# Performance work log

Hardware: AMD Instinct MI355X
Metric: run time of the kernel (lower is better)

## Reference

```python
import jax, jax.numpy as jnp
import numpy as np

B, T, D, H = 2, 2048, 2048, 16
HD = D // H  # head_dim = 128
NEG = -1e9


def setup_inputs() -> dict:
    key = jax.random.key(0)
    k1, k2, k3 = jax.random.split(key, 3)
    x = jax.random.normal(k1, (B, T, D), dtype=jnp.float32)
    # additive causal mask: 0 on/below diagonal, large negative above
    mask = jnp.where(jnp.tril(jnp.ones((T, T), dtype=bool)), 0.0, NEG).astype(jnp.float32)
    causal_mask = mask[None, None]  # [1,1,T,T]
    w_qkv = jax.random.normal(k2, (3 * D, D), dtype=jnp.float32) * (D ** -0.5)
    w_out = jax.random.normal(k3, (D, D), dtype=jnp.float32) * (D ** -0.5)
    b_out = jnp.zeros((D,), dtype=jnp.float32)
    return {"x": x, "causal_mask": causal_mask, "w_qkv": w_qkv, "w_out": w_out, "b_out": b_out}


def reference(x, causal_mask, w_qkv, w_out, b_out):
    scale = HD ** -0.5
    qkv = jnp.einsum('btd,ed->bte', x, w_qkv)          # [B,T,3D]
    q, k, v = jnp.split(qkv, 3, axis=-1)
    def heads(t):  # [B,T,D] -> [B,H,T,HD]
        return t.reshape(B, T, H, HD).transpose(0, 2, 1, 3)
    q, k, v = heads(q), heads(k), heads(v)
    attn = jnp.einsum('bhqd,bhkd->bhqk', q, k) * scale + causal_mask
    attn = jax.nn.softmax(attn, axis=-1)
    out = jnp.einsum('bhqk,bhkd->bhqd', attn, v)       # [B,H,T,HD]
    out = out.transpose(0, 2, 1, 3).reshape(B, T, D)
    return jnp.einsum('btd,ed->bte', out, w_out) + b_out
```

## Files before the change

kernel.cpp:

```cpp
#include <hip/hip_runtime.h>
#include <stdint.h>

typedef uint16_t u16;
typedef __attribute__((ext_vector_type(8))) short short8;
typedef __attribute__((ext_vector_type(4))) float f32x4;
typedef __attribute__((ext_vector_type(16))) float f32x16;

#define MFMA16(a, b, c) __builtin_amdgcn_mfma_f32_16x16x32_bf16((a), (b), (c), 0, 0, 0)
#define MFMA32(a, b, c) __builtin_amdgcn_mfma_f32_32x32x16_bf16((a), (b), (c), 0, 0, 0)
#define AS1 __attribute__((address_space(1)))
#define AS3 __attribute__((address_space(3)))

__device__ __forceinline__ void gld_lds16(const u16* g, u16* l) {
  __builtin_amdgcn_global_load_lds((const AS1 void*)g, (AS3 void*)l, 16, 0, 0);
}

__device__ __forceinline__ u16 f2bf(float f) {
  uint32_t u = __float_as_uint(f);
  u += 0x7fffu + ((u >> 16) & 1u);
  return (u16)(u >> 16);
}

__global__ __launch_bounds__(256) void cvt_all(const float* __restrict__ x,
                                               const float* __restrict__ wqkv,
                                               const float* __restrict__ wout,
                                               u16* __restrict__ xb,
                                               u16* __restrict__ wqkvb,
                                               u16* __restrict__ woutb) {
  const int n1 = 8388608 / 4, n2 = 12582912 / 4;
  int i = blockIdx.x * 256 + threadIdx.x;
  const float* src;
  u16* dst;
  int j;
  if (i < n1) {
    src = x; dst = xb; j = i;
  } else if (i < n1 + n2) {
    src = wqkv; dst = wqkvb; j = i - n1;
  } else {
    src = wout; dst = woutb; j = i - n1 - n2;
  }
  float4 v = ((const float4*)src)[j];
  uint2 o;
  o.x = (uint32_t)f2bf(v.x) | ((uint32_t)f2bf(v.y) << 16);
  o.y = (uint32_t)f2bf(v.z) | ((uint32_t)f2bf(v.w) << 16);
  ((uint2*)dst)[j] = o;
}

template <int N>
__device__ __forceinline__ void bar_vm() {
  asm volatile("s_waitcnt vmcnt(%0)\n\ts_barrier" ::"n"(N) : "memory");
}
__device__ __forceinline__ void bar_fence() {
  asm volatile("s_barrier" ::: "memory");
}

__global__ __launch_bounds__(512, 2) void proj8_gemm(const u16* __restrict__ xb,
                                                     const u16* __restrict__ wqkvb,
                                                     u16* __restrict__ qkb) {
  constexpr int ASZ = 256 * 64;
  constexpr int NT = 32;
  __shared__ u16 sm[4 * ASZ];

  int bx = blockIdx.x;
  bx = (bx & 7) * 32 + (bx >> 3);
  const int mt = bx >> 4, nt = bx & 15;
  const u16* Ab = xb + (size_t)mt * 256 * 2048;
  const u16* Bb = wqkvb + (size_t)nt * 256 * 2048;
  u16* C = qkb + (size_t)mt * 256 * 4096 + nt * 256;

  const int tid = threadIdx.x, lane = tid & 63, w = tid >> 6;
  const int wm = w >> 2, wn = w & 3;
  const int lo = lane & 15, q4 = lane >> 4;

  f32x4 acc[8][4];
  const f32x4 fzero = {0.f, 0.f, 0.f, 0.f};
#pragma unroll
  for (int i = 0; i < 8; ++i)
#pragma unroll
    for (int j = 0; j < 4; ++j) acc[i][j] = fzero;

  auto stage_half = [&](int tau, int h) {
    const int slot = tau & 1;
    const int k0 = tau * 64;
    const u16* G = (h < 2) ? Bb : Ab;
    u16* L = sm + (h < 2 ? 2 * ASZ : 0) + slot * ASZ;
#pragma unroll
    for (int s = 0; s < 2; ++s) {
      const int c = tid + s * 512;
      const int hr = c >> 3, pc = c & 7;
      const int r = (h < 2) ? (h * 128 + hr)
                            : ((hr & 63) + ((hr >> 6) << 7) + ((h & 1) << 6));
      const int c4 = pc ^ (r & 7);
      gld_lds16(G + (size_t)r * 2048 + k0 + c4 * 8, L + r * 64 + pc * 8);
    }
  };

  stage_half(0, 0);
  stage_half(0, 1);
  stage_half(0, 2);
  stage_half(0, 3);
  bar_vm<2>();

  for (int tau = 0; tau < NT; ++tau) {
    const u16* As = sm + (tau & 1) * ASZ;
    const u16* Bs = sm + 2 * ASZ + (tau & 1) * ASZ;
    short8 bf[8];
#pragma unroll
    for (int q = 0; q < 4; ++q) {
      if (q == 0) {
#pragma unroll
        for (int j = 0; j < 4; ++j)
#pragma unroll
          for (int kk = 0; kk < 2; ++kk) {
            const int r = wn * 64 + j * 16 + lo;
            bf[j * 2 + kk] =
                *(const short8*)(Bs + r * 64 + (((kk * 4 + q4) ^ (r & 7)) * 8));
          }
      }
      short8 af[2][2];
#pragma unroll
      for (int i = 0; i < 2; ++i)
#pragma unroll
        for (int kk = 0; kk < 2; ++kk) {
          const int r = wm * 128 + q * 32 + i * 16 + lo;
          af[i][kk] =
              *(const short8*)(As + r * 64 + (((kk * 4 + q4) ^ (r & 7)) * 8));
        }
      if (tau + 1 < NT) stage_half(tau + 1, q);
      bar_fence();
      __builtin_amdgcn_s_setprio(1);
#pragma unroll
      for (int i = 0; i < 2; ++i)
#pragma unroll
        for (int j = 0; j < 4; ++j)
#pragma unroll
          for (int kk = 0; kk < 2; ++kk)
            acc[q * 2 + i][j] = MFMA16(af[i][kk], bf[j * 2 + kk], acc[q * 2 + i][j]);
      __builtin_amdgcn_s_setprio(0);
      if (q == 0) {
        if (tau == NT - 1) bar_vm<0>();
        else bar_vm<2>();
      } else if (q == 1) {
        bar_vm<4>();
      } else if (q == 2) {
        bar_vm<6>();
      } else {
        if (tau < NT - 1) bar_vm<2>();
      }
    }
  }

#pragma unroll
  for (int i = 0; i < 8; ++i)
#pragma unroll
    for (int j = 0; j < 4; ++j) {
      const int col = wn * 64 + j * 16 + lo;
#pragma unroll
      for (int e = 0; e < 4; ++e) {
        const int row = wm * 128 + i * 16 + q4 * 4 + e;
        C[(size_t)row * 4096 + col] = f2bf(acc[i][j][e]);
      }
    }
}

template <int MFR>
__device__ __forceinline__ void gemm_core3(const u16* __restrict__ Ab,
                                           const u16* __restrict__ Bb,
                                           u16* sm, int tid,
                                           f32x4 acc[MFR][4]) {
  constexpr int AROWS = MFR * 32;
  constexpr int ASZ = AROWS * 32;
  constexpr int BSZ = 128 * 32;
  constexpr int BUF = ASZ + BSZ;
  constexpr int NT = 64;
  constexpr int ALD = AROWS / 64;
  constexpr int VN = ALD + 2;

  const int lane = tid & 63, w = tid >> 6;
  const int wr = w >> 1, wc = w & 1;
  const int lo = lane & 15, q4 = lane >> 4;
  const int pcl = (((lo & 1) << 2) | q4) ^ ((lo >> 1) & 7);
  const int loff = (lo >> 1) * 64 + pcl * 8;

  auto stage = [&](int g) {
    u16* As = sm + (g % 3) * BUF;
    u16* Bs = As + ASZ;
    const int k0 = g * 32;
#pragma unroll
    for (int s = 0; s < ALD; ++s) {
      const int c = tid + s * 256;
      const int sr = c >> 3, pc = c & 7;
      const int t = pc ^ (sr & 7);
      const int r = sr * 2 + (t >> 2), c4 = t & 3;
      gld_lds16(Ab + (size_t)r * 2048 + k0 + c4 * 8, As + c * 8);
    }
#pragma unroll
    for (int s = 0; s < 2; ++s) {
      const int c = tid + s * 256;
      const int sr = c >> 3, pc = c & 7;
      const int t = pc ^ (sr & 7);
      const int r = sr * 2 + (t >> 2), c4 = t & 3;
      gld_lds16(Bb + (size_t)r * 2048 + k0 + c4 * 8, Bs + c * 8);
    }
  };

  stage(0);
  stage(1);
  bar_vm<VN>();

  for (int g = 0; g < NT; ++g) {
    const u16* As = sm + (g % 3) * BUF;
    const u16* Bs = As + ASZ;
    if (g + 2 < NT) stage(g + 2);
    short8 af[MFR], bf[4];
#pragma unroll
    for (int i = 0; i < MFR; ++i)
      af[i] = *(const short8*)(As + (wr * (MFR * 16) + i * 16) * 32 + loff);
#pragma unroll
    for (int j = 0; j < 4; ++j)
      bf[j] = *(const short8*)(Bs + (wc * 64 + j * 16) * 32 + loff);
    __builtin_amdgcn_s_setprio(1);
#pragma unroll
    for (int i = 0; i < MFR; ++i)
#pragma unroll
      for (int j = 0; j < 4; ++j) acc[i][j] = MFMA16(af[i], bf[j], acc[i][j]);
    __builtin_amdgcn_s_setprio(0);
    if (g + 1 < NT) {
      if (g + 2 < NT) {
        bar_vm<VN>();
      } else {
        bar_vm<0>();
      }
    }
  }
}

__global__ __launch_bounds__(256, 2) void vproj_gemm(const u16* __restrict__ wqkvb,
                                                     const u16* __restrict__ xb,
                                                     u16* __restrict__ vtb) {
  __shared__ u16 sm[3 * (256 * 32 + 128 * 32)];
  int bx = blockIdx.x;
  bx = (bx & 7) * 32 + (bx >> 3);
  const int tid = threadIdx.x;
  const int mt = bx >> 5, nt = bx & 31;
  const u16* Ab = wqkvb + (size_t)(4096 + mt * 256) * 2048;
  const u16* Bb = xb + (size_t)nt * 128 * 2048;
  u16* C = vtb + (size_t)mt * 256 * 4096 + nt * 128;
  f32x4 acc[8][4];
  const f32x4 fzero = {0.f, 0.f, 0.f, 0.f};
#pragma unroll
  for (int i = 0; i < 8; ++i)
#pragma unroll
    for (int j = 0; j < 4; ++j) acc[i][j] = fzero;

  gemm_core3<8>(Ab, Bb, sm, tid, acc);

  const int lane = tid & 63, w = tid >> 6;
  const int wr = w >> 1, wc = w & 1;
  const int lo = lane & 15, q4 = lane >> 4;
#pragma unroll
  for (int i = 0; i < 8; ++i)
#pragma unroll
    for (int j = 0; j < 4; ++j) {
      const int col = wc * 64 + j * 16 + lo;
#pragma unroll
      for (int e = 0; e < 4; ++e) {
        const int row = wr * 128 + i * 16 + q4 * 4 + e;
        C[(size_t)row * 4096 + col] = f2bf(acc[i][j][e]);
      }
    }
}

__global__ __launch_bounds__(256, 2) void out_gemm(const u16* __restrict__ A,
                                                   const u16* __restrict__ B,
                                                   float* __restrict__ Cf,
                                                   const float* __restrict__ bias) {
  __shared__ u16 sm[3 * (256 * 32 + 128 * 32)];
  int bx = blockIdx.x;
  bx = (bx & 7) * 32 + (bx >> 3);
  const int tid = threadIdx.x;
  const int mt = bx >> 4, nt = bx & 15;
  const u16* Ab = A + (size_t)mt * 256 * 2048;
  const u16* Bb = B + (size_t)nt * 128 * 2048;
  f32x4 acc[8][4];
  const f32x4 fzero = {0.f, 0.f, 0.f, 0.f};
#pragma unroll
  for (int i = 0; i < 8; ++i)
#pragma unroll
    for (int j = 0; j < 4; ++j) acc[i][j] = fzero;

  gemm_core3<8>(Ab, Bb, sm, tid, acc);

  const int lane = tid & 63, w = tid >> 6;
  const int wr = w >> 1, wc = w & 1;
  const int lo = lane & 15, q4 = lane >> 4;
#pragma unroll
  for (int i = 0; i < 8; ++i)
#pragma unroll
    for (int j = 0; j < 4; ++j) {
      const int col = nt * 128 + wc * 64 + j * 16 + lo;
      const float bv = bias[col];
#pragma unroll
      for (int e = 0; e < 4; ++e) {
        const int row = mt * 256 + wr * 128 + i * 16 + q4 * 4 + e;
        Cf[(size_t)row * 2048 + col] = acc[i][j][e] + bv;
      }
    }
}

__device__ __forceinline__ int swz(int r, int c) {
  return r * 128 + (c ^ (((r ^ (r >> 3)) & 7) << 4));
}

__global__ __launch_bounds__(512) void flash_attn(const u16* __restrict__ qk,
                                                  const u16* __restrict__ vt,
                                                  u16* __restrict__ aout) {
  constexpr int T = 2048, WQK = 4096, D = 2048;
  constexpr int TILE = 128 * 128;
  __shared__ u16 smem[5 * TILE];

  const int bx = blockIdx.x;
  const int p = bx >> 5;
  const int g = bx & 31;
  const int h = g & 15, b = g >> 4;
  const int tid = threadIdx.x, lane = tid & 63, w = tid >> 6;
  const int wr = w >> 1, wcc = w & 1;
  const int l31 = lane & 31, h5 = lane >> 5;

  const u16* Qb = qk + (size_t)b * T * WQK + h * 128;
  const u16* Kb = Qb + 2048;
  const u16* Vtb = vt + (size_t)h * 128 * 4096 + b * 2048;
  u16* Ps = smem + 4 * TILE;

  const float cexp = 0.08838834764831843f * 1.4426950408889634f;
  short8 onesf;
#pragma unroll
  for (int j = 0; j < 8; ++j) onesf[j] = (short)0x3F80;

  for (int half = 0; half < 2; ++half) {
    const int qt = half ? p : 15 - p;
    const int q0 = qt * 128;

    short8 qf[8];
#pragma unroll
    for (int kc = 0; kc < 8; ++kc)
      qf[kc] = *(const short8*)(Qb + (size_t)(q0 + wr * 32 + l31) * WQK +
                                kc * 16 + h5 * 8);

    f32x16 o[2], osum;
#pragma unroll
    for (int e = 0; e < 16; ++e) { o[0][e] = 0.f; o[1][e] = 0.f; osum[e] = 0.f; }

    __syncthreads();
#pragma unroll
    for (int s = 0; s < 4; ++s) {
      const int c = tid + s * 512, r = c >> 4, cc = c & 15;
      const int cs = cc ^ (((r ^ (r >> 3)) & 7) << 1);
      gld_lds16(Kb + (size_t)r * WQK + cs * 8, smem + c * 8);
      gld_lds16(Vtb + (size_t)r * 4096 + cs * 8, smem + 2 * TILE + c * 8);
    }

    for (int kt = 0; kt <= qt; ++kt) {
      const int curo = (kt & 1) * TILE, nxto = TILE - curo;
      __syncthreads();
      if (kt < qt) {
        const int k0n = (kt + 1) * 128;
#pragma unroll
        for (int s = 0; s < 4; ++s) {
          const int c = tid + s * 512, r = c >> 4, cc = c & 15;
          const int cs = cc ^ (((r ^ (r >> 3)) & 7) << 1);
          gld_lds16(Kb + (size_t)(k0n + r) * WQK + cs * 8, smem + nxto + c * 8);
          gld_lds16(Vtb + (size_t)r * 4096 + k0n + cs * 8,
                    smem + 2 * TILE + nxto + c * 8);
        }
      }

      const u16* Ksc = smem + curo;
      const u16* Vsc = smem + 2 * TILE + curo;

      f32x16 s2[2];
#pragma unroll
      for (int e = 0; e < 16; ++e) { s2[0][e] = 0.f; s2[1][e] = 0.f; }
#pragma unroll
      for (int kc = 0; kc < 8; ++kc)
#pragma unroll
        for (int ct = 0; ct < 2; ++ct) {
          short8 kf = *(const short8*)&Ksc[swz(wcc * 64 + ct * 32 + l31,
                                               kc * 16 + h5 * 8)];
          s2[ct] = MFMA32(qf[kc], kf, s2[ct]);
        }

      const bool diag = (kt == qt);
#pragma unroll
      for (int ct = 0; ct < 2; ++ct) {
        const int kcol = wcc * 64 + ct * 32 + l31;
#pragma unroll
        for (int reg = 0; reg < 16; ++reg) {
          const int qrow = wr * 32 + (reg & 3) + 8 * (reg >> 2) + 4 * h5;
          float pv = exp2f(s2[ct][reg] * cexp);
          if (diag && (kcol > qrow)) pv = 0.f;
          Ps[swz(qrow, kcol)] = f2bf(pv);
        }
      }
      asm volatile("s_waitcnt lgkmcnt(0)\n\ts_barrier" ::: "memory");

#pragma unroll
      for (int kc = 0; kc < 8; ++kc) {
        short8 pa = *(const short8*)&Ps[swz(wr * 32 + l31, kc * 16 + h5 * 8)];
        osum = MFMA32(pa, onesf, osum);
#pragma unroll
        for (int dt = 0; dt < 2; ++dt) {
          short8 vf = *(const short8*)&Vsc[swz(wcc * 64 + dt * 32 + l31,
                                               kc * 16 + h5 * 8)];
          o[dt] = MFMA32(pa, vf, o[dt]);
        }
      }
    }

#pragma unroll
    for (int reg = 0; reg < 16; ++reg) {
      const int row = q0 + wr * 32 + (reg & 3) + 8 * (reg >> 2) + 4 * h5;
      const float inv = 1.f / osum[reg];
#pragma unroll
      for (int dt = 0; dt < 2; ++dt)
        aout[(size_t)(b * T + row) * D + h * 128 + wcc * 64 + dt * 32 + l31] =
            f2bf(o[dt][reg] * inv);
    }
  }
}

extern "C" void kernel_launch(void* const* d_in, const int* in_sizes, int n_in,
                              void* d_out, int out_size, void* d_ws, size_t ws_size,
                              hipStream_t stream) {
  const float* x = (const float*)d_in[0];
  const float* w_qkv = (const float*)d_in[2];
  const float* w_out = (const float*)d_in[3];
  const float* b_out = (const float*)d_in[4];
  float* out = (float*)d_out;

  const int BT = 4096, D = 2048, D3 = 6144;
  u16* xb = (u16*)d_ws;
  u16* wqkvb = xb + (size_t)BT * D;
  u16* woutb = wqkvb + (size_t)D3 * D;
  u16* qkb = woutb + (size_t)D * D;
  u16* vtb = qkb + (size_t)BT * 4096;
  u16* attnb = vtb + (size_t)D * BT;

  const int total4 = (BT * D + D3 * D + D * D) / 4;
  cvt_all<<<total4 / 256, 256, 0, stream>>>(x, w_qkv, w_out, xb, wqkvb, woutb);
  proj8_gemm<<<256, 512, 0, stream>>>(xb, wqkvb, qkb);
  vproj_gemm<<<256, 256, 0, stream>>>(wqkvb, xb, vtb);
  flash_attn<<<256, 512, 0, stream>>>(qkb, vtb, attnb);
  out_gemm<<<256, 256, 0, stream>>>(attnb, woutb, out, b_out);
}
```

Baseline: 355.9 us.

## Keep softmax probabilities in registers, fold scale into Q projection, shrink GEMM tiles

```diff
diff --git a/kernel.cpp b/kernel.cpp
--- a/kernel.cpp
+++ b/kernel.cpp
@@ -150,6 +150,8 @@
     }
   }
 
+  const float sc =
+      (nt < 8) ? (0.08838834764831843f * 1.4426950408889634f) : 1.0f;
 #pragma unroll
   for (int i = 0; i < 8; ++i)
 #pragma unroll
@@ -158,7 +160,7 @@
 #pragma unroll
       for (int e = 0; e < 4; ++e) {
         const int row = wm * 128 + i * 16 + q4 * 4 + e;
-        C[(size_t)row * 4096 + col] = f2bf(acc[i][j][e]);
+        C[(size_t)row * 4096 + col] = f2bf(acc[i][j][e] * sc);
       }
     }
 }
@@ -238,34 +240,34 @@
 __global__ __launch_bounds__(256, 2) void vproj_gemm(const u16* __restrict__ wqkvb,
                                                      const u16* __restrict__ xb,
                                                      u16* __restrict__ vtb) {
-  __shared__ u16 sm[3 * (256 * 32 + 128 * 32)];
+  __shared__ u16 sm[3 * (128 * 32 + 128 * 32)];
   int bx = blockIdx.x;
-  bx = (bx & 7) * 32 + (bx >> 3);
+  bx = (bx & 7) * 64 + (bx >> 3);
   const int tid = threadIdx.x;
   const int mt = bx >> 5, nt = bx & 31;
-  const u16* Ab = wqkvb + (size_t)(4096 + mt * 256) * 2048;
+  const u16* Ab = wqkvb + (size_t)(4096 + mt * 128) * 2048;
   const u16* Bb = xb + (size_t)nt * 128 * 2048;
-  u16* C = vtb + (size_t)mt * 256 * 4096 + nt * 128;
-  f32x4 acc[8][4];
+  u16* C = vtb + (size_t)mt * 128 * 4096 + nt * 128;
+  f32x4 acc[4][4];
   const f32x4 fzero = {0.f, 0.f, 0.f, 0.f};
 #pragma unroll
-  for (int i = 0; i < 8; ++i)
+  for (int i = 0; i < 4; ++i)
 #pragma unroll
     for (int j = 0; j < 4; ++j) acc[i][j] = fzero;
 
-  gemm_core3<8>(Ab, Bb, sm, tid, acc);
+  gemm_core3<4>(Ab, Bb, sm, tid, acc);
 
   const int lane = tid & 63, w = tid >> 6;
   const int wr = w >> 1, wc = w & 1;
   const int lo = lane & 15, q4 = lane >> 4;
 #pragma unroll
-  for (int i = 0; i < 8; ++i)
+  for (int i = 0; i < 4; ++i)
 #pragma unroll
     for (int j = 0; j < 4; ++j) {
       const int col = wc * 64 + j * 16 + lo;
 #pragma unroll
       for (int e = 0; e < 4; ++e) {
-        const int row = wr * 128 + i * 16 + q4 * 4 + e;
+        const int row = wr * 64 + i * 16 + q4 * 4 + e;
         C[(size_t)row * 4096 + col] = f2bf(acc[i][j][e]);
       }
     }
@@ -275,34 +277,34 @@
                                                    const u16* __restrict__ B,
                                                    float* __restrict__ Cf,
                                                    const float* __restrict__ bias) {
-  __shared__ u16 sm[3 * (256 * 32 + 128 * 32)];
+  __shared__ u16 sm[3 * (128 * 32 + 128 * 32)];
   int bx = blockIdx.x;
-  bx = (bx & 7) * 32 + (bx >> 3);
+  bx = (bx & 7) * 64 + (bx >> 3);
   const int tid = threadIdx.x;
   const int mt = bx >> 4, nt = bx & 15;
-  const u16* Ab = A + (size_t)mt * 256 * 2048;
+  const u16* Ab = A + (size_t)mt * 128 * 2048;
   const u16* Bb = B + (size_t)nt * 128 * 2048;
-  f32x4 acc[8][4];
+  f32x4 acc[4][4];
   const f32x4 fzero = {0.f, 0.f, 0.f, 0.f};
 #pragma unroll
-  for (int i = 0; i < 8; ++i)
+  for (int i = 0; i < 4; ++i)
 #pragma unroll
     for (int j = 0; j < 4; ++j) acc[i][j] = fzero;
 
-  gemm_core3<8>(Ab, Bb, sm, tid, acc);
+  gemm_core3<4>(Ab, Bb, sm, tid, acc);
 
   const int lane = tid & 63, w = tid >> 6;
   const int wr = w >> 1, wc = w & 1;
   const int lo = lane & 15, q4 = lane >> 4;
 #pragma unroll
-  for (int i = 0; i < 8; ++i)
+  for (int i = 0; i < 4; ++i)
 #pragma unroll
     for (int j = 0; j < 4; ++j) {
       const int col = nt * 128 + wc * 64 + j * 16 + lo;
       const float bv = bias[col];
 #pragma unroll
       for (int e = 0; e < 4; ++e) {
-        const int row = mt * 256 + wr * 128 + i * 16 + q4 * 4 + e;
+        const int row = mt * 128 + wr * 64 + i * 16 + q4 * 4 + e;
         Cf[(size_t)row * 2048 + col] = acc[i][j][e] + bv;
       }
     }
@@ -317,25 +319,20 @@
                                                   u16* __restrict__ aout) {
   constexpr int T = 2048, WQK = 4096, D = 2048;
   constexpr int TILE = 128 * 128;
-  __shared__ u16 smem[5 * TILE];
+  __shared__ u16 smem[4 * TILE];
 
   const int bx = blockIdx.x;
   const int p = bx >> 5;
   const int g = bx & 31;
   const int h = g & 15, b = g >> 4;
   const int tid = threadIdx.x, lane = tid & 63, w = tid >> 6;
-  const int wr = w >> 1, wcc = w & 1;
-  const int l31 = lane & 31, h5 = lane >> 5;
+  const int wr = w & 3, wk = w >> 2;
+  const int l31 = lane & 31, hi = lane >> 5;
 
   const u16* Qb = qk + (size_t)b * T * WQK + h * 128;
   const u16* Kb = Qb + 2048;
   const u16* Vtb = vt + (size_t)h * 128 * 4096 + b * 2048;
-  u16* Ps = smem + 4 * TILE;
-
-  const float cexp = 0.08838834764831843f * 1.4426950408889634f;
-  short8 onesf;
-#pragma unroll
-  for (int j = 0; j < 8; ++j) onesf[j] = (short)0x3F80;
+  float* fex = (float*)smem;
 
   for (int half = 0; half < 2; ++half) {
     const int qt = half ? p : 15 - p;
@@ -345,11 +342,14 @@
 #pragma unroll
     for (int kc = 0; kc < 8; ++kc)
       qf[kc] = *(const short8*)(Qb + (size_t)(q0 + wr * 32 + l31) * WQK +
-                                kc * 16 + h5 * 8);
-
-    f32x16 o[2], osum;
-#pragma unroll
-    for (int e = 0; e < 16; ++e) { o[0][e] = 0.f; o[1][e] = 0.f; osum[e] = 0.f; }
+                                kc * 16 + hi * 8);
+
+    f32x16 o[4];
+    float osum = 0.f;
+#pragma unroll
+    for (int dt = 0; dt < 4; ++dt)
+#pragma unroll
+      for (int e = 0; e < 16; ++e) o[dt][e] = 0.f;
 
     __syncthreads();
 #pragma unroll
@@ -385,46 +385,83 @@
       for (int kc = 0; kc < 8; ++kc)
 #pragma unroll
         for (int ct = 0; ct < 2; ++ct) {
-          short8 kf = *(const short8*)&Ksc[swz(wcc * 64 + ct * 32 + l31,
-                                               kc * 16 + h5 * 8)];
-          s2[ct] = MFMA32(qf[kc], kf, s2[ct]);
+          short8 kf = *(const short8*)&Ksc[swz(wk * 64 + ct * 32 + l31,
+                                               kc * 16 + hi * 8)];
+          s2[ct] = MFMA32(kf, qf[kc], s2[ct]);
         }
 
       const bool diag = (kt == qt);
 #pragma unroll
       for (int ct = 0; ct < 2; ++ct) {
-        const int kcol = wcc * 64 + ct * 32 + l31;
-#pragma unroll
-        for (int reg = 0; reg < 16; ++reg) {
-          const int qrow = wr * 32 + (reg & 3) + 8 * (reg >> 2) + 4 * h5;
-          float pv = exp2f(s2[ct][reg] * cexp);
-          if (diag && (kcol > qrow)) pv = 0.f;
-          Ps[swz(qrow, kcol)] = f2bf(pv);
-        }
-      }
-      asm volatile("s_waitcnt lgkmcnt(0)\n\ts_barrier" ::: "memory");
-
-#pragma unroll
-      for (int kc = 0; kc < 8; ++kc) {
-        short8 pa = *(const short8*)&Ps[swz(wr * 32 + l31, kc * 16 + h5 * 8)];
-        osum = MFMA32(pa, onesf, osum);
-#pragma unroll
-        for (int dt = 0; dt < 2; ++dt) {
-          short8 vf = *(const short8*)&Vsc[swz(wcc * 64 + dt * 32 + l31,
-                                               kc * 16 + h5 * 8)];
-          o[dt] = MFMA32(pa, vf, o[dt]);
-        }
-      }
-    }
-
-#pragma unroll
-    for (int reg = 0; reg < 16; ++reg) {
-      const int row = q0 + wr * 32 + (reg & 3) + 8 * (reg >> 2) + 4 * h5;
-      const float inv = 1.f / osum[reg];
-#pragma unroll
-      for (int dt = 0; dt < 2; ++dt)
-        aout[(size_t)(b * T + row) * D + h * 128 + wcc * 64 + dt * 32 + l31] =
-            f2bf(o[dt][reg] * inv);
+        float pv[16];
+#pragma unroll
+        for (int r = 0; r < 16; ++r) {
+          float e = exp2f(s2[ct][r]);
+          if (diag) {
+            const int kcol = wk * 64 + ct * 32 + (r & 3) + 8 * (r >> 2) + 4 * hi;
+            const int qrow = wr * 32 + l31;
+            if (kcol > qrow) e = 0.f;
+          }
+          pv[r] = e;
+          osum += e;
+        }
+        short8 pa2[2];
+#pragma unroll
+        for (int ks2 = 0; ks2 < 2; ++ks2) {
+          uint32_t y0, y1, y2, y3;
+          asm("v_cvt_pk_bf16_f32 %0, %1, %2"
+              : "=v"(y0) : "v"(pv[ks2 * 8 + 0]), "v"(pv[ks2 * 8 + 1]));
+          asm("v_cvt_pk_bf16_f32 %0, %1, %2"
+              : "=v"(y1) : "v"(pv[ks2 * 8 + 2]), "v"(pv[ks2 * 8 + 3]));
+          asm("v_cvt_pk_bf16_f32 %0, %1, %2"
+              : "=v"(y2) : "v"(pv[ks2 * 8 + 4]), "v"(pv[ks2 * 8 + 5]));
+          asm("v_cvt_pk_bf16_f32 %0, %1, %2"
+              : "=v"(y3) : "v"(pv[ks2 * 8 + 6]), "v"(pv[ks2 * 8 + 7]));
+          asm volatile("v_permlane32_swap_b32 %0, %1" : "+v"(y0), "+v"(y2));
+          asm volatile("v_permlane32_swap_b32 %0, %1" : "+v"(y1), "+v"(y3));
+          int4 t4;
+          t4.x = (int)y0; t4.y = (int)y1; t4.z = (int)y2; t4.w = (int)y3;
+          pa2[ks2] = *(short8*)&t4;
+        }
+#pragma unroll
+        for (int ks2 = 0; ks2 < 2; ++ks2) {
+          const int ksg = ct * 2 + ks2;
+#pragma unroll
+          for (int dt = 0; dt < 4; ++dt) {
+            short8 vf = *(const short8*)&Vsc[swz(dt * 32 + l31,
+                                                 wk * 64 + ksg * 16 + hi * 8)];
+            o[dt] = MFMA32(pa2[ks2], vf, o[dt]);
+          }
+        }
+      }
+    }
+
+    const float osum_full = osum + __shfl_xor(osum, 32);
+    __syncthreads();
+    if (wk == 1) {
+#pragma unroll
+      for (int dt = 0; dt < 4; ++dt)
+#pragma unroll
+        for (int r = 0; r < 16; ++r) {
+          const int qr = wr * 32 + (r & 3) + 8 * (r >> 2) + 4 * hi;
+          fex[qr * 128 + dt * 32 + l31] = o[dt][r];
+        }
+    }
+    if (hi == 0) fex[16384 + wk * 128 + wr * 32 + l31] = osum_full;
+    __syncthreads();
+    if (wk == 0) {
+#pragma unroll
+      for (int r = 0; r < 16; ++r) {
+        const int qr = wr * 32 + (r & 3) + 8 * (r >> 2) + 4 * hi;
+        const float st = fex[16384 + qr] + fex[16384 + 128 + qr];
+        const float inv = 1.f / st;
+#pragma unroll
+        for (int dt = 0; dt < 4; ++dt) {
+          const float v = o[dt][r] + fex[qr * 128 + dt * 32 + l31];
+          aout[(size_t)(b * T + q0 + qr) * D + h * 128 + dt * 32 + l31] =
+              f2bf(v * inv);
+        }
+      }
     }
   }
 }
@@ -449,7 +486,7 @@
   const int total4 = (BT * D + D3 * D + D * D) / 4;
   cvt_all<<<total4 / 256, 256, 0, stream>>>(x, w_qkv, w_out, xb, wqkvb, woutb);
   proj8_gemm<<<256, 512, 0, stream>>>(xb, wqkvb, qkb);
-  vproj_gemm<<<256, 256, 0, stream>>>(wqkvb, xb, vtb);
+  vproj_gemm<<<512, 256, 0, stream>>>(wqkvb, xb, vtb);
   flash_attn<<<256, 512, 0, stream>>>(qkb, vtb, attnb);
-  out_gemm<<<256, 256, 0, stream>>>(attnb, woutb, out, b_out);
-}
+  out_gemm<<<512, 256, 0, stream>>>(attnb, woutb, out, b_out);
+}
```

Result: faster. 338.4 us (-4.9%).
